# Kernel tuning notes

Hardware: AMD Instinct MI355X
Metric: run time of the kernel (lower is better)

## Reference

```python
import jax, jax.numpy as jnp
import numpy as np

B, T, S, H, V = 2, 512, 400, 1024, 50257


def setup_inputs() -> dict:
    key = jax.random.key(0)
    ks = jax.random.split(key, 5)
    x = jax.random.normal(ks[0], (B, T, H), dtype=jnp.float32)
    attn_dist = jax.random.normal(ks[1], (B, T, S), dtype=jnp.float32)
    enc_batch_extend_vocab = jax.random.randint(ks[2], (B, S), 0, V)
    # learned params of nn.Linear(H, V) and nn.Linear(H, 1)
    proj_w = jax.random.normal(ks[3], (V, H), dtype=jnp.float32) * 0.02
    proj_b = jnp.zeros((V,), dtype=jnp.float32)
    pgen_w = jax.random.normal(ks[4], (1, H), dtype=jnp.float32) * 0.02
    pgen_b = jnp.zeros((1,), dtype=jnp.float32)
    return {
        "x": x,
        "attn_dist": attn_dist,
        "enc_batch_extend_vocab": enc_batch_extend_vocab,
        "temp": 1,
        "proj_w": proj_w,
        "proj_b": proj_b,
        "pgen_w": pgen_w,
        "pgen_b": pgen_b,
    }


def reference(x, attn_dist, enc_batch_extend_vocab, temp, proj_w, proj_b, pgen_w, pgen_b):
    # p_gen gate: sigmoid(Linear(H -> 1))  -> [B, T, 1]
    p_gen = jax.nn.sigmoid(jnp.einsum("bth,oh->bto", x, pgen_w) + pgen_b)
    # vocab projection: [B, T, V]
    logit = jnp.einsum("bth,vh->btv", x, proj_w) + proj_b
    vocab_dist = jax.nn.softmax(logit / temp, axis=2)
    vocab_dist_ = p_gen * vocab_dist  # [B, T, V]
    # copy distribution over source tokens: [B, T, S]
    attn = jax.nn.softmax(attn_dist / temp, axis=-1)
    attn_ = (1.0 - p_gen) * attn
    # scatter_add along vocab dim; source ids broadcast over decode steps
    idx = jnp.broadcast_to(enc_batch_extend_vocab[:, None, :], attn_.shape)  # [B, T, S]
    scat = jax.vmap(jax.vmap(lambda vd, ix, a: vd.at[ix].add(a)))
    out = scat(vocab_dist_, idx, attn_)
    return jnp.log(out + 1e-40)
```

## Files before the change

### kernel.cpp

```cpp
#include <hip/hip_runtime.h>
#include <hip/hip_bf16.h>

#define BB 2
#define TT 512
#define SS 400
#define HH 1024
#define VV 50257
#define MM (BB*TT)

#define NTILE 393
#define NT_PAD 400
#define VPAD 50304

typedef __attribute__((ext_vector_type(8))) short short8;
typedef __attribute__((ext_vector_type(4))) float f32x4;

#define AS1 __attribute__((address_space(1)))
#define AS3 __attribute__((address_space(3)))

static __device__ __forceinline__ void gl_lds16(const unsigned short* g, unsigned short* l) {
    __builtin_amdgcn_global_load_lds((const AS1 unsigned int*)(g), (AS3 unsigned int*)(l), 16, 0, 0);
}

static __device__ __forceinline__ unsigned short f2bf(float f) {
    union { float f; unsigned u; } x;
    x.f = f;
    unsigned r = x.u + 0x7FFFu + ((x.u >> 16) & 1u);
    return (unsigned short)(r >> 16);
}

static __device__ __forceinline__ float get_invtemp(const int* tp) {
    int iv = *tp;
    float f;
    if (iv > 0 && iv < 100000) f = (float)iv;
    else                       f = __int_as_float(iv);
    return 1.0f / f;
}

__global__ void zero2_k(int* a, int na, int* b, int nb) {
    int i = blockIdx.x * blockDim.x + threadIdx.x;
    int st = gridDim.x * blockDim.x;
    for (int t = i; t < na; t += st) a[t] = 0;
    for (int t = i; t < nb; t += st) b[t] = 0;
}

__global__ void cvt_x_k(const float* __restrict__ x, unsigned short* __restrict__ xb) {
    int i = blockIdx.x * 256 + threadIdx.x;
    float4 v = ((const float4*)x)[i];
    ushort4 o;
    o.x = f2bf(v.x); o.y = f2bf(v.y); o.z = f2bf(v.z); o.w = f2bf(v.w);
    ((ushort4*)xb)[i] = o;
}

__global__ void cvt_w_k(const float* __restrict__ W, unsigned short* __restrict__ Wb) {
    size_t g = (size_t)blockIdx.x * 256 + threadIdx.x;
    size_t e0 = g * 8;
    int v = (int)(e0 >> 10);
    short8 o;
    if (v < VV) {
        float4 a = *(const float4*)(W + e0);
        float4 b = *(const float4*)(W + e0 + 4);
        o[0] = f2bf(a.x); o[1] = f2bf(a.y); o[2] = f2bf(a.z); o[3] = f2bf(a.w);
        o[4] = f2bf(b.x); o[5] = f2bf(b.y); o[6] = f2bf(b.z); o[7] = f2bf(b.w);
    } else {
        o = (short8){0,0,0,0,0,0,0,0};
    }
    *(short8*)(Wb + e0) = o;
}

__global__ void pgen_k(const float* __restrict__ x, const float* __restrict__ pw,
                       const float* __restrict__ pb, float* __restrict__ pgen) {
    int m = blockIdx.x, tid = threadIdx.x;
    float s = 0.f;
    for (int h = tid; h < HH; h += 256) s += x[(size_t)m * HH + h] * pw[h];
    for (int off = 32; off; off >>= 1) s += __shfl_down(s, off);
    __shared__ float red[4];
    if ((tid & 63) == 0) red[tid >> 6] = s;
    __syncthreads();
    if (tid == 0) {
        float t = red[0] + red[1] + red[2] + red[3] + pb[0];
        pgen[m] = 1.0f / (1.0f + __expf(-t));
    }
}

__global__ void map_build_k(const int* __restrict__ enc, int* __restrict__ mapv) {
    int t = blockIdx.x * blockDim.x + threadIdx.x;
    if (t >= BB * SS) return;
    int b = t / SS, s = t % SS;
    int id = enc[b * SS + s];
    atomicCAS(&mapv[(size_t)b * VV + id], 0, s + 1);
}

__global__ void attn_k(const float* __restrict__ attn, const int* __restrict__ enc,
                       const int* __restrict__ mapv, const float* __restrict__ pgen,
                       float* __restrict__ Aacc, const int* __restrict__ tempp) {
    int m = blockIdx.x, tid = threadIdx.x;
    int b = m >> 9;
    float invt = get_invtemp(tempp);
    __shared__ float sv[SS];
    __shared__ float red[256];
    float loc = -1e30f;
    for (int s = tid; s < SS; s += 256) {
        float v = attn[(size_t)m * SS + s] * invt;
        sv[s] = v;
        loc = fmaxf(loc, v);
    }
    red[tid] = loc; __syncthreads();
    for (int h = 128; h; h >>= 1) { if (tid < h) red[tid] = fmaxf(red[tid], red[tid + h]); __syncthreads(); }
    float mx = red[0]; __syncthreads();
    float ls = 0.f;
    for (int s = tid; s < SS; s += 256) ls += __expf(sv[s] - mx);
    red[tid] = ls; __syncthreads();
    for (int h = 128; h; h >>= 1) { if (tid < h) red[tid] += red[tid + h]; __syncthreads(); }
    float scale = (1.0f - pgen[m]) / red[0];
    for (int s = tid; s < SS; s += 256) {
        int id = enc[b * SS + s];
        int s0 = mapv[(size_t)b * VV + id] - 1;
        atomicAdd(&Aacc[(size_t)m * SS + s0], __expf(sv[s] - mx) * scale);
    }
}

__global__ __launch_bounds__(256) void gemm2_k(
    const unsigned short* __restrict__ xb, const unsigned short* __restrict__ Wb,
    const float* __restrict__ bias, float* __restrict__ out) {
    __shared__ unsigned short As[128 * 64];
    __shared__ unsigned short Bs[128 * 64];

    int wgid = blockIdx.x;
    int xcd = wgid & 7;
    int l = wgid >> 3;
    int nt = xcd * 50 + (l >> 3);
    int mt = l & 7;
    if (nt >= NTILE) return;
    int m0 = mt * 128, n0 = nt * 128;

    int tid = threadIdx.x;
    int lane = tid & 63, w = tid >> 6;
    int wr = w >> 1, wc = w & 1;
    int r15 = lane & 15, kg = lane >> 4;

    size_t aoff[4], boff[4];
#pragma unroll
    for (int i = 0; i < 4; i++) {
        int q = i * 256 + tid;
        int row = q >> 3;
        int jc = (q & 7) ^ (row & 7);
        aoff[i] = (size_t)(m0 + row) * HH + jc * 8;
        boff[i] = (size_t)(n0 + row) * HH + jc * 8;
    }

    f32x4 acc[4][4];
#pragma unroll
    for (int i = 0; i < 4; i++)
#pragma unroll
        for (int j = 0; j < 4; j++) acc[i][j] = (f32x4){0.f, 0.f, 0.f, 0.f};

    for (int kt = 0; kt < HH / 64; ++kt) {
        int k0 = kt * 64;
#pragma unroll
        for (int i = 0; i < 4; i++) {
            gl_lds16(xb + aoff[i] + k0, As + (i * 256 + w * 64) * 8);
            gl_lds16(Wb + boff[i] + k0, Bs + (i * 256 + w * 64) * 8);
        }
        __syncthreads();
#pragma unroll
        for (int h = 0; h < 2; h++) {
            short8 af[4], bf[4];
#pragma unroll
            for (int mi = 0; mi < 4; mi++) {
                int row = wr * 64 + mi * 16 + r15;
                int jc = ((h << 2) | kg) ^ (row & 7);
                af[mi] = *(const short8*)&As[row * 64 + jc * 8];
            }
#pragma unroll
            for (int ni = 0; ni < 4; ni++) {
                int row = wc * 64 + ni * 16 + r15;
                int jc = ((h << 2) | kg) ^ (row & 7);
                bf[ni] = *(const short8*)&Bs[row * 64 + jc * 8];
            }
#pragma unroll
            for (int mi = 0; mi < 4; mi++)
#pragma unroll
                for (int ni = 0; ni < 4; ni++)
                    acc[mi][ni] = __builtin_amdgcn_mfma_f32_16x16x32_bf16(af[mi], bf[ni], acc[mi][ni], 0, 0, 0);
        }
        __syncthreads();
    }

#pragma unroll
    for (int ni = 0; ni < 4; ni++) {
        int gn = n0 + wc * 64 + ni * 16 + r15;
        if (gn < VV) {
            float bv = bias[gn];
#pragma unroll
            for (int mi = 0; mi < 4; mi++) {
                int gmb = m0 + wr * 64 + mi * 16 + (kg << 2);
#pragma unroll
                for (int j = 0; j < 4; j++)
                    out[(size_t)(gmb + j) * VV + gn] = acc[mi][ni][j] + bv;
            }
        }
    }
}

__global__ __launch_bounds__(256) void gemm_old_k(
    const unsigned short* __restrict__ xb, const float* __restrict__ W,
    const float* __restrict__ bias, float* __restrict__ out) {
    __shared__ unsigned short As[128][40];
    __shared__ unsigned short Bs[128][40];
    int bid = blockIdx.x;
    int mt = bid & 7;
    int nt = bid >> 3;
    int m0 = mt * 128, n0 = nt * 128;
    int tid = threadIdx.x;
    int lid = tid & 63, w = tid >> 6;
    int wr = w >> 1, wc = w & 1;
    int row16 = lid & 15, kg = lid >> 4;

    f32x4 acc[4][4];
#pragma unroll
    for (int i = 0; i < 4; i++)
#pragma unroll
        for (int j = 0; j < 4; j++) acc[i][j] = (f32x4){0.f, 0.f, 0.f, 0.f};

    int tr = tid >> 3;
    int tc = (tid & 7) << 2;

    for (int kt = 0; kt < HH / 32; ++kt) {
        int k0 = kt * 32;
        __syncthreads();
#pragma unroll
        for (int i = 0; i < 4; i++) {
            int r = tr + 32 * i;
            ushort4 a4 = *(const ushort4*)&xb[(size_t)(m0 + r) * HH + k0 + tc];
            *(ushort4*)&As[r][tc] = a4;
            int v = n0 + r; v = (v < VV) ? v : (VV - 1);
            float4 w4 = *(const float4*)&W[(size_t)v * HH + k0 + tc];
            ushort4 b4;
            b4.x = f2bf(w4.x); b4.y = f2bf(w4.y); b4.z = f2bf(w4.z); b4.w = f2bf(w4.w);
            *(ushort4*)&Bs[r][tc] = b4;
        }
        __syncthreads();
        short8 af[4], bf[4];
#pragma unroll
        for (int i = 0; i < 4; i++) {
            af[i] = *(const short8*)&As[wr * 64 + i * 16 + row16][kg * 8];
            bf[i] = *(const short8*)&Bs[wc * 64 + i * 16 + row16][kg * 8];
        }
#pragma unroll
        for (int mi = 0; mi < 4; mi++)
#pragma unroll
            for (int ni = 0; ni < 4; ni++)
                acc[mi][ni] = __builtin_amdgcn_mfma_f32_16x16x32_bf16(af[mi], bf[ni], acc[mi][ni], 0, 0, 0);
    }
#pragma unroll
    for (int ni = 0; ni < 4; ni++) {
        int gn = n0 + wc * 64 + ni * 16 + row16;
        if (gn < VV) {
            float bv = bias[gn];
#pragma unroll
            for (int mi = 0; mi < 4; mi++) {
                int gmb = m0 + wr * 64 + mi * 16 + (kg << 2);
#pragma unroll
                for (int j = 0; j < 4; j++)
                    out[(size_t)(gmb + j) * VV + gn] = acc[mi][ni][j] + bv;
            }
        }
    }
}

__global__ void rowreduce_k(const float* __restrict__ out, float* __restrict__ lse,
                            const int* __restrict__ tempp) {
    int m = blockIdx.x, tid = threadIdx.x;
    float invt = get_invtemp(tempp);
    const float* row = out + (size_t)m * VV;
    int sk = (-m) & 3;
    int nchunk = (VV - sk) >> 2;
    float mi = -1e30f, si = 0.f;
    for (int c = tid; c < nchunk; c += 256) {
        float4 x4 = *(const float4*)(row + sk + 4 * c);
        float xs[4] = {x4.x, x4.y, x4.z, x4.w};
#pragma unroll
        for (int j = 0; j < 4; j++) {
            float x = xs[j] * invt;
            float nm = fmaxf(mi, x);
            si = si * __expf(mi - nm) + __expf(x - nm);
            mi = nm;
        }
    }
    if (tid == 0) {
        for (int v = 0; v < sk; v++) {
            float x = row[v] * invt;
            float nm = fmaxf(mi, x);
            si = si * __expf(mi - nm) + __expf(x - nm);
            mi = nm;
        }
        for (int v = sk + 4 * nchunk; v < VV; v++) {
            float x = row[v] * invt;
            float nm = fmaxf(mi, x);
            si = si * __expf(mi - nm) + __expf(x - nm);
            mi = nm;
        }
    }
    __shared__ float sm[256], ss[256];
    sm[tid] = mi; ss[tid] = si; __syncthreads();
    for (int h = 128; h; h >>= 1) {
        if (tid < h) {
            float m2 = sm[tid + h], s2 = ss[tid + h];
            float nm = fmaxf(sm[tid], m2);
            ss[tid] = ss[tid] * __expf(sm[tid] - nm) + s2 * __expf(m2 - nm);
            sm[tid] = nm;
        }
        __syncthreads();
    }
    if (tid == 0) lse[m] = sm[0] + __logf(ss[0]);
}

__global__ void finalize_k(float* __restrict__ out, const float* __restrict__ pgen,
                           const float* __restrict__ lse, const int* __restrict__ mapv,
                           const float* __restrict__ Aacc, const int* __restrict__ tempp) {
    int m = blockIdx.y;
    int b = m >> 9;
    float invt = get_invtemp(tempp);
    float pg = pgen[m], L = lse[m];
    size_t base = (size_t)m * VV;
    const int* mrow = mapv + (size_t)b * VV;
    const float* arow = Aacc + (size_t)m * SS;
    int sk = (-m) & 3;
    int nchunk = (VV - sk) >> 2;
    int c = blockIdx.x * 256 + threadIdx.x;
    if (c < nchunk) {
        int v0 = sk + 4 * c;
        float4 l4 = *(const float4*)(out + base + v0);
        float xs[4] = {l4.x, l4.y, l4.z, l4.w};
        float rs[4];
#pragma unroll
        for (int j = 0; j < 4; j++) {
            float p = pg * __expf(xs[j] * invt - L);
            int jm = mrow[v0 + j];
            if (jm) p += arow[jm - 1];
            rs[j] = __logf(p + 1e-40f);
        }
        float4 o4 = {rs[0], rs[1], rs[2], rs[3]};
        *(float4*)(out + base + v0) = o4;
    }
    if (blockIdx.x == 0 && threadIdx.x == 0) {
        for (int v = 0; v < sk; v++) {
            float p = pg * __expf(out[base + v] * invt - L);
            int jm = mrow[v];
            if (jm) p += arow[jm - 1];
            out[base + v] = __logf(p + 1e-40f);
        }
        for (int v = sk + 4 * nchunk; v < VV; v++) {
            float p = pg * __expf(out[base + v] * invt - L);
            int jm = mrow[v];
            if (jm) p += arow[jm - 1];
            out[base + v] = __logf(p + 1e-40f);
        }
    }
}

extern "C" void kernel_launch(void* const* d_in, const int* in_sizes, int n_in,
                              void* d_out, int out_size, void* d_ws, size_t ws_size,
                              hipStream_t stream) {
    const float* x      = (const float*)d_in[0];
    const float* attn   = (const float*)d_in[1];
    const int*   enc    = (const int*)d_in[2];
    const int*   temp   = (const int*)d_in[3];
    const float* proj_w = (const float*)d_in[4];
    const float* proj_b = (const float*)d_in[5];
    const float* pgen_w = (const float*)d_in[6];
    const float* pgen_b = (const float*)d_in[7];
    float* out = (float*)d_out;

    char* ws = (char*)d_ws;
    const size_t WB_BYTES = (size_t)VPAD * HH * 2;

    size_t o_wb   = 0;
    size_t o_xb   = o_wb + WB_BYTES;
    size_t o_pgen = o_xb + 2097152;
    size_t o_lse  = o_pgen + 4096;
    size_t o_map  = o_lse + 4096;
    size_t o_aacc = o_map + 402432;
    size_t need   = o_aacc + (size_t)MM * SS * 4;

    if (ws_size >= need) {
        unsigned short* wb   = (unsigned short*)(ws + o_wb);
        unsigned short* xb   = (unsigned short*)(ws + o_xb);
        float*          pgen = (float*)(ws + o_pgen);
        float*          lse  = (float*)(ws + o_lse);
        int*            mapv = (int*)(ws + o_map);
        float*          Aacc = (float*)(ws + o_aacc);

        zero2_k<<<512, 256, 0, stream>>>(mapv, BB * VV, (int*)Aacc, MM * SS);
        cvt_x_k<<<1024, 256, 0, stream>>>(x, xb);
        cvt_w_k<<<(VPAD * HH / 8 + 255) / 256, 256, 0, stream>>>(proj_w, wb);
        pgen_k<<<MM, 256, 0, stream>>>(x, pgen_w, pgen_b, pgen);
        map_build_k<<<4, 256, 0, stream>>>(enc, mapv);
        attn_k<<<MM, 256, 0, stream>>>(attn, enc, mapv, pgen, Aacc, temp);
        gemm2_k<<<8 * NT_PAD, 256, 0, stream>>>(xb, wb, proj_b, out);
        rowreduce_k<<<MM, 256, 0, stream>>>(out, lse, temp);
        finalize_k<<<dim3(50, MM), 256, 0, stream>>>(out, pgen, lse, mapv, Aacc, temp);
    } else {
        unsigned short* xb   = (unsigned short*)(ws + 0);
        float*          pgen = (float*)(ws + 2097152);
        float*          lse  = (float*)(ws + 2101248);
        int*            mapv = (int*)(ws + 2105344);
        float*          Aacc = (float*)(ws + 2507776);

        zero2_k<<<512, 256, 0, stream>>>(mapv, BB * VV, (int*)Aacc, MM * SS);
        cvt_x_k<<<1024, 256, 0, stream>>>(x, xb);
        pgen_k<<<MM, 256, 0, stream>>>(x, pgen_w, pgen_b, pgen);
        map_build_k<<<4, 256, 0, stream>>>(enc, mapv);
        attn_k<<<MM, 256, 0, stream>>>(attn, enc, mapv, pgen, Aacc, temp);
        gemm_old_k<<<8 * NTILE, 256, 0, stream>>>(xb, proj_w, proj_b, out);
        rowreduce_k<<<MM, 256, 0, stream>>>(out, lse, temp);
        finalize_k<<<dim3(50, MM), 256, 0, stream>>>(out, pgen, lse, mapv, Aacc, temp);
    }
}
```

Measured before the change: 447.3 us.

## Fuse softmax max/sum partials into GEMM epilogue and double-buffer LDS tiles

The GEMM epilogue now computes per-tile online-softmax max and sum for each row and writes them to small partial buffers. A tiny combine kernel merges these into the log-sum-exp, which removes the separate row-reduce pass that re-read the whole 1024x50257 logit matrix. The GEMM main loop is also double-buffered in LDS, so the next K-tile load is issued before computing on the current one. This doubles LDS usage and adds exp and shuffle work to the epilogue. The combine kernel runs only 1024 threads serially over 393 tiles.

```diff
diff --git a/kernel.cpp b/kernel.cpp
--- a/kernel.cpp
+++ b/kernel.cpp
@@ -120,11 +120,15 @@
     }
 }
 
-__global__ __launch_bounds__(256) void gemm2_k(
+__global__ __launch_bounds__(256) void gemm3_k(
     const unsigned short* __restrict__ xb, const unsigned short* __restrict__ Wb,
-    const float* __restrict__ bias, float* __restrict__ out) {
-    __shared__ unsigned short As[128 * 64];
-    __shared__ unsigned short Bs[128 * 64];
+    const float* __restrict__ bias, float* __restrict__ out,
+    float* __restrict__ pmax, float* __restrict__ psum,
+    const int* __restrict__ tempp) {
+    __shared__ unsigned short As[2 * 128 * 64];
+    __shared__ unsigned short Bs[2 * 128 * 64];
+    __shared__ float red_mx[2][2][64];
+    __shared__ float red_sm[2][2][64];
 
     int wgid = blockIdx.x;
     int xcd = wgid & 7;
@@ -155,14 +159,25 @@
 #pragma unroll
         for (int j = 0; j < 4; j++) acc[i][j] = (f32x4){0.f, 0.f, 0.f, 0.f};
 
+#pragma unroll
+    for (int i = 0; i < 4; i++) {
+        gl_lds16(xb + aoff[i], As + (i * 256 + w * 64) * 8);
+        gl_lds16(Wb + boff[i], Bs + (i * 256 + w * 64) * 8);
+    }
+    __syncthreads();
+
+    int cur = 0;
     for (int kt = 0; kt < HH / 64; ++kt) {
-        int k0 = kt * 64;
-#pragma unroll
-        for (int i = 0; i < 4; i++) {
-            gl_lds16(xb + aoff[i] + k0, As + (i * 256 + w * 64) * 8);
-            gl_lds16(Wb + boff[i] + k0, Bs + (i * 256 + w * 64) * 8);
-        }
-        __syncthreads();
+        if (kt + 1 < HH / 64) {
+            int k0 = (kt + 1) * 64;
+            int nb = (cur ^ 1) * 8192;
+#pragma unroll
+            for (int i = 0; i < 4; i++) {
+                gl_lds16(xb + aoff[i] + k0, As + nb + (i * 256 + w * 64) * 8);
+                gl_lds16(Wb + boff[i] + k0, Bs + nb + (i * 256 + w * 64) * 8);
+            }
+        }
+        int cb = cur * 8192;
 #pragma unroll
         for (int h = 0; h < 2; h++) {
             short8 af[4], bf[4];
@@ -170,13 +185,13 @@
             for (int mi = 0; mi < 4; mi++) {
                 int row = wr * 64 + mi * 16 + r15;
                 int jc = ((h << 2) | kg) ^ (row & 7);
-                af[mi] = *(const short8*)&As[row * 64 + jc * 8];
+                af[mi] = *(const short8*)&As[cb + row * 64 + jc * 8];
             }
 #pragma unroll
             for (int ni = 0; ni < 4; ni++) {
                 int row = wc * 64 + ni * 16 + r15;
                 int jc = ((h << 2) | kg) ^ (row & 7);
-                bf[ni] = *(const short8*)&Bs[row * 64 + jc * 8];
+                bf[ni] = *(const short8*)&Bs[cb + row * 64 + jc * 8];
             }
 #pragma unroll
             for (int mi = 0; mi < 4; mi++)
@@ -185,22 +200,82 @@
                     acc[mi][ni] = __builtin_amdgcn_mfma_f32_16x16x32_bf16(af[mi], bf[ni], acc[mi][ni], 0, 0, 0);
         }
         __syncthreads();
-    }
-
+        cur ^= 1;
+    }
+
+    float invt = get_invtemp(tempp);
+    float bv[4]; bool vld[4]; int gn[4];
 #pragma unroll
     for (int ni = 0; ni < 4; ni++) {
-        int gn = n0 + wc * 64 + ni * 16 + r15;
-        if (gn < VV) {
-            float bv = bias[gn];
+        gn[ni] = n0 + wc * 64 + ni * 16 + r15;
+        vld[ni] = gn[ni] < VV;
+        bv[ni] = vld[ni] ? bias[gn[ni]] : 0.f;
+    }
+#pragma unroll
+    for (int mi = 0; mi < 4; mi++) {
+#pragma unroll
+        for (int j = 0; j < 4; j++) {
+            float mx = -1e30f;
+#pragma unroll
+            for (int ni = 0; ni < 4; ni++)
+                if (vld[ni]) mx = fmaxf(mx, (acc[mi][ni][j] + bv[ni]) * invt);
+            float sm = 0.f;
+#pragma unroll
+            for (int ni = 0; ni < 4; ni++)
+                if (vld[ni]) sm += __expf((acc[mi][ni][j] + bv[ni]) * invt - mx);
+#pragma unroll
+            for (int o = 1; o < 16; o <<= 1) {
+                float m2 = __shfl_xor(mx, o);
+                float s2 = __shfl_xor(sm, o);
+                float nm = fmaxf(mx, m2);
+                sm = sm * __expf(mx - nm) + s2 * __expf(m2 - nm);
+                mx = nm;
+            }
+            if (r15 == 0) {
+                red_mx[wr][wc][mi * 16 + kg * 4 + j] = mx;
+                red_sm[wr][wc][mi * 16 + kg * 4 + j] = sm;
+            }
+        }
+    }
+#pragma unroll
+    for (int ni = 0; ni < 4; ni++) {
+        if (vld[ni]) {
 #pragma unroll
             for (int mi = 0; mi < 4; mi++) {
                 int gmb = m0 + wr * 64 + mi * 16 + (kg << 2);
 #pragma unroll
                 for (int j = 0; j < 4; j++)
-                    out[(size_t)(gmb + j) * VV + gn] = acc[mi][ni][j] + bv;
-            }
-        }
-    }
+                    out[(size_t)(gmb + j) * VV + gn[ni]] = acc[mi][ni][j] + bv[ni];
+            }
+        }
+    }
+    __syncthreads();
+    if (tid < 128) {
+        int r = tid & 63, wr2 = tid >> 6;
+        float m1 = red_mx[wr2][0][r], s1 = red_sm[wr2][0][r];
+        float m2 = red_mx[wr2][1][r], s2 = red_sm[wr2][1][r];
+        float nm = fmaxf(m1, m2);
+        float s = s1 * __expf(m1 - nm) + s2 * __expf(m2 - nm);
+        int gm = m0 + wr2 * 64 + r;
+        pmax[(size_t)gm * NT_PAD + nt] = nm;
+        psum[(size_t)gm * NT_PAD + nt] = s;
+    }
+}
+
+__global__ void lse_combine_k(const float* __restrict__ pmax, const float* __restrict__ psum,
+                              float* __restrict__ lse) {
+    int m = blockIdx.x * 128 + threadIdx.x;
+    if (m >= MM) return;
+    const float* pm = pmax + (size_t)m * NT_PAD;
+    const float* ps = psum + (size_t)m * NT_PAD;
+    float M = -1e30f, S = 0.f;
+    for (int t = 0; t < NTILE; ++t) {
+        float m2 = pm[t], s2 = ps[t];
+        float nm = fmaxf(M, m2);
+        S = S * __expf(M - nm) + s2 * __expf(m2 - nm);
+        M = nm;
+    }
+    lse[m] = M + __logf(S);
 }
 
 __global__ __launch_bounds__(256) void gemm_old_k(
@@ -255,15 +330,15 @@
     }
 #pragma unroll
     for (int ni = 0; ni < 4; ni++) {
-        int gn = n0 + wc * 64 + ni * 16 + row16;
-        if (gn < VV) {
-            float bv = bias[gn];
+        int gnv = n0 + wc * 64 + ni * 16 + row16;
+        if (gnv < VV) {
+            float bvv = bias[gnv];
 #pragma unroll
             for (int mi = 0; mi < 4; mi++) {
                 int gmb = m0 + wr * 64 + mi * 16 + (kg << 2);
 #pragma unroll
                 for (int j = 0; j < 4; j++)
-                    out[(size_t)(gmb + j) * VV + gn] = acc[mi][ni][j] + bv;
+                    out[(size_t)(gmb + j) * VV + gnv] = acc[mi][ni][j] + bvv;
             }
         }
     }
@@ -382,7 +457,9 @@
     size_t o_lse  = o_pgen + 4096;
     size_t o_map  = o_lse + 4096;
     size_t o_aacc = o_map + 402432;
-    size_t need   = o_aacc + (size_t)MM * SS * 4;
+    size_t o_pmax = o_aacc + (size_t)MM * SS * 4;
+    size_t o_psum = o_pmax + (size_t)MM * NT_PAD * 4;
+    size_t need   = o_psum + (size_t)MM * NT_PAD * 4;
 
     if (ws_size >= need) {
         unsigned short* wb   = (unsigned short*)(ws + o_wb);
@@ -391,6 +468,8 @@
         float*          lse  = (float*)(ws + o_lse);
         int*            mapv = (int*)(ws + o_map);
         float*          Aacc = (float*)(ws + o_aacc);
+        float*          pmax = (float*)(ws + o_pmax);
+        float*          psum = (float*)(ws + o_psum);
 
         zero2_k<<<512, 256, 0, stream>>>(mapv, BB * VV, (int*)Aacc, MM * SS);
         cvt_x_k<<<1024, 256, 0, stream>>>(x, xb);
@@ -398,8 +477,8 @@
         pgen_k<<<MM, 256, 0, stream>>>(x, pgen_w, pgen_b, pgen);
         map_build_k<<<4, 256, 0, stream>>>(enc, mapv);
         attn_k<<<MM, 256, 0, stream>>>(attn, enc, mapv, pgen, Aacc, temp);
-        gemm2_k<<<8 * NT_PAD, 256, 0, stream>>>(xb, wb, proj_b, out);
-        rowreduce_k<<<MM, 256, 0, stream>>>(out, lse, temp);
+        gemm3_k<<<8 * NT_PAD, 256, 0, stream>>>(xb, wb, proj_b, out, pmax, psum, temp);
+        lse_combine_k<<<8, 128, 0, stream>>>(pmax, psum, lse);
         finalize_k<<<dim3(50, MM), 256, 0, stream>>>(out, pgen, lse, mapv, Aacc, temp);
     } else {
         unsigned short* xb   = (unsigned short*)(ws + 0);
```

Result: slower. 528.6 us (+18.2%).
